# Performance work log

Hardware: AMD Instinct MI355X
Metric: run time of the kernel (lower is better)

Reference implementation:

```python
import jax, jax.numpy as jnp
import numpy as np

HEADS = 4
DIM_HEAD = 32
CHUNK = 1024
GROUPS = 8
EPS = 1e-5


def setup_inputs() -> dict:
    key = jax.random.key(0)
    k1, k2, k3 = jax.random.split(key, 3)
    b, dim, h, w = 8, 64, 96, 96
    inner = HEADS * DIM_HEAD  # 128
    x = jax.random.normal(k1, (b, dim, h, w), dtype=jnp.float32)
    W_qkv = jax.random.normal(k2, (3 * inner, dim), dtype=jnp.float32) * (1.0 / np.sqrt(dim))
    W_out = jax.random.normal(k3, (dim, inner), dtype=jnp.float32) * (1.0 / np.sqrt(inner))
    b_out = jnp.zeros((dim,), dtype=jnp.float32)
    gamma = jnp.ones((dim,), dtype=jnp.float32)
    beta = jnp.zeros((dim,), dtype=jnp.float32)
    return {"x": x, "W_qkv": W_qkv, "W_out": W_out, "b_out": b_out,
            "gamma": gamma, "beta": beta}


def reference(x, W_qkv, W_out, b_out, gamma, beta):
    b, c, h, w = x.shape
    n = h * w
    nch = n // CHUNK  # number of full chunks (n chosen divisible by CHUNK)
    d = DIM_HEAD
    BH = b * HEADS

    # 1x1 conv (no bias) == matmul over channel dim
    xf = x.reshape(b, c, n)
    qkv = jnp.einsum('oc,bcn->bon', W_qkv, xf)          # [b, 3*inner, n]
    q, k, v = jnp.split(qkv, 3, axis=1)                  # each [b, inner, n]

    def chunkify(t):
        # [b, inner, n] -> [BH, nch, d, CHUNK]; slicing i:i+CHUNK on last axis
        # equals reshaping n -> (nch, CHUNK) in order.
        return t.reshape(BH, d, nch, CHUNK).transpose(0, 2, 1, 3)

    qc, kc, vc = chunkify(q), chunkify(k), chunkify(v)

    qs = jax.nn.softmax(qc, axis=-1)  # softmax over chunk spatial positions
    ks = jax.nn.softmax(kc, axis=-2)  # softmax over head channels

    # context = k_chunk^T @ v_chunk : [BH, nch, CHUNK, CHUNK]
    ctx = jnp.einsum('gkdi,gkdj->gkij', ks, vc)
    # chunk_out = q_chunk @ context : [BH, nch, d, CHUNK]
    out = jnp.einsum('gkdi,gkij->gkdj', qs, ctx)

    # concat chunks back along spatial dim, reshape to image layout
    out = out.transpose(0, 2, 1, 3).reshape(b, HEADS * d, h, w)

    # to_out: 1x1 conv with bias, then GroupNorm(8, dim)
    y = jnp.einsum('oc,bchw->bohw', W_out, out) + b_out[None, :, None, None]

    yg = y.reshape(b, GROUPS, c // GROUPS, h, w)
    mu = jnp.mean(yg, axis=(2, 3, 4), keepdims=True)
    var = jnp.var(yg, axis=(2, 3, 4), keepdims=True)
    yn = ((yg - mu) * jax.lax.rsqrt(var + EPS)).reshape(b, c, h, w)
    return yn * gamma[None, :, None, None] + beta[None, :, None, None]
```

## Files before the change

kernel.cpp:

```cpp
#include <hip/hip_runtime.h>
#include <hip/hip_bf16.h>

#define N_POS 9216
#define NCHUNK 9
#define BATCH 8
#define CDIM 64
#define HEADS 4
#define EPS 1e-5f

#define PPART_SZ ((size_t)32 * NCHUNK * 1024)
#define NPART 8
#define UBF_BYTES ((size_t)BATCH * NCHUNK * 64 * 128 * 2)
#define WBF_BYTES ((size_t)384 * 64 * 2)

typedef __attribute__((ext_vector_type(8))) short short8;
typedef __attribute__((ext_vector_type(4))) float f32x4;

static __device__ inline unsigned pk2(float a, float b) {
    __hip_bfloat162 h2(__float2bfloat16(a), __float2bfloat16(b));
    return *reinterpret_cast<unsigned*>(&h2);
}
static __device__ inline float bf2f(short s) {
    union { unsigned u; float f; } c; c.u = ((unsigned)(unsigned short)s) << 16; return c.f;
}

__global__ __launch_bounds__(256) void wprep_kernel(const float* __restrict__ Wqkv,
        __hip_bfloat16* __restrict__ wbf, float* __restrict__ stats) {
    int i = blockIdx.x * 256 + threadIdx.x;
    if (i < 6144) {
        float4 v = ((const float4*)Wqkv)[i];
        uint2 u; u.x = pk2(v.x, v.y); u.y = pk2(v.z, v.w);
        ((uint2*)wbf)[i] = u;
    }
    if (i < 128) stats[i] = 0.f;
}

__global__ __launch_bounds__(256) void qkp_kernel(const float* __restrict__ x,
        const __hip_bfloat16* __restrict__ wbf, float* __restrict__ Pparts) {
    int bx = blockIdx.x;
    int b  = blockIdx.y;
    int ck = bx >> 3, pt = bx & 7;
    __shared__ __align__(16) char lraw[36864];
    __hip_bfloat16 (*xs)[72]  = (__hip_bfloat16(*)[72])lraw;
    __hip_bfloat16 (*skT)[72] = (__hip_bfloat16(*)[72])lraw;
    int t = threadIdx.x, w = t >> 6, l = t & 63;
    int l15 = l & 15, quad = l >> 4;

    f32x4 pac[2][2];
    pac[0][0] = (f32x4){0,0,0,0}; pac[0][1] = (f32x4){0,0,0,0};
    pac[1][0] = (f32x4){0,0,0,0}; pac[1][1] = (f32x4){0,0,0,0};

    for (int half = 0; half < 2; ++half) {
        int n0 = bx * 128 + half * 64;
        {
            int p = t & 63, cbase = (t >> 6) * 16;
            const float* xb = x + (size_t)b * CDIM * N_POS + n0 + p;
            #pragma unroll
            for (int j = 0; j < 16; j += 4) {
                float v0 = xb[(size_t)(cbase + j + 0) * N_POS];
                float v1 = xb[(size_t)(cbase + j + 1) * N_POS];
                float v2 = xb[(size_t)(cbase + j + 2) * N_POS];
                float v3 = xb[(size_t)(cbase + j + 3) * N_POS];
                uint2 u; u.x = pk2(v0, v1); u.y = pk2(v2, v3);
                *reinterpret_cast<uint2*>(&xs[p][cbase + j]) = u;
            }
        }
        __syncthreads();

        f32x4 acc[4][4];
        #pragma unroll
        for (int mt = 0; mt < 4; ++mt)
            #pragma unroll
            for (int nt = 0; nt < 4; ++nt) acc[mt][nt] = (f32x4){0.f, 0.f, 0.f, 0.f};
        #pragma unroll
        for (int ks = 0; ks < 2; ++ks) {
            int k0 = ks * 32 + quad * 8;
            short8 av[4];
            #pragma unroll
            for (int mt = 0; mt < 4; ++mt)
                av[mt] = *reinterpret_cast<const short8*>(&xs[mt * 16 + l15][k0]);
            #pragma unroll
            for (int nt = 0; nt < 4; ++nt) {
                short8 bw = *reinterpret_cast<const short8*>(wbf + (size_t)(w * 64 + nt * 16 + l15) * 64 + k0);
                #pragma unroll
                for (int mt = 0; mt < 4; ++mt)
                    acc[mt][nt] = __builtin_amdgcn_mfma_f32_16x16x32_bf16(av[mt], bw, acc[mt][nt], 0, 0, 0);
            }
        }
        __syncthreads();

        if (w < 2) {
            #pragma unroll
            for (int nt = 0; nt < 4; ++nt) {
                int ch = w * 64 + nt * 16 + l15;
                #pragma unroll
                for (int mt = 0; mt < 4; ++mt) {
                    uint2 u;
                    u.x = pk2(__expf(acc[mt][nt][0]), __expf(acc[mt][nt][1]));
                    u.y = pk2(__expf(acc[mt][nt][2]), __expf(acc[mt][nt][3]));
                    *reinterpret_cast<uint2*>(&skT[ch][mt * 16 + quad * 4]) = u;
                }
            }
        } else {
            #pragma unroll
            for (int nt = 0; nt < 4; ++nt) {
                int ch = w * 64 + nt * 16 + l15;
                #pragma unroll
                for (int mt = 0; mt < 4; ++mt) {
                    uint2 u;
                    u.x = pk2(acc[mt][nt][0], acc[mt][nt][1]);
                    u.y = pk2(acc[mt][nt][2], acc[mt][nt][3]);
                    *reinterpret_cast<uint2*>(&skT[ch][mt * 16 + quad * 4]) = u;
                }
            }
        }
        __syncthreads();

        {
            int p = t & 63, h = t >> 6;
            float kr[32]; float mx = -1e30f;
            #pragma unroll
            for (int d = 0; d < 32; ++d) { kr[d] = bf2f(*(const short*)&skT[128 + h * 32 + d][p]); mx = fmaxf(mx, kr[d]); }
            float s = 0.f;
            #pragma unroll
            for (int d = 0; d < 32; ++d) { kr[d] = __expf(kr[d] - mx); s += kr[d]; }
            float is = 1.f / s;
            #pragma unroll
            for (int d = 0; d < 32; ++d) skT[128 + h * 32 + d][p] = __float2bfloat16(kr[d] * is);
        }
        __syncthreads();

        #pragma unroll
        for (int step = 0; step < 2; ++step) {
            int k0 = step * 32 + quad * 8;
            short8 bk[2];
            #pragma unroll
            for (int nt = 0; nt < 2; ++nt)
                bk[nt] = *reinterpret_cast<const short8*>(&skT[128 + w * 32 + nt * 16 + l15][k0]);
            #pragma unroll
            for (int mt = 0; mt < 2; ++mt) {
                short8 aq = *reinterpret_cast<const short8*>(&skT[w * 32 + mt * 16 + l15][k0]);
                pac[mt][0] = __builtin_amdgcn_mfma_f32_16x16x32_bf16(aq, bk[0], pac[mt][0], 0, 0, 0);
                pac[mt][1] = __builtin_amdgcn_mfma_f32_16x16x32_bf16(aq, bk[1], pac[mt][1], 0, 0, 0);
            }
        }
        __syncthreads();
    }

    float* Pp = Pparts + (size_t)pt * PPART_SZ + ((size_t)(b * 4 + w) * NCHUNK + ck) * 1024;
    #pragma unroll
    for (int mt = 0; mt < 2; ++mt)
        #pragma unroll
        for (int nt = 0; nt < 2; ++nt)
            #pragma unroll
            for (int r = 0; r < 4; ++r)
                Pp[(mt * 16 + quad * 4 + r) * 32 + nt * 16 + l15] = pac[mt][nt][r];
}

__global__ __launch_bounds__(256) void umat_kernel(const float* __restrict__ Wout,
        const float* __restrict__ Pparts, __hip_bfloat16* __restrict__ Ubf) {
    int ck = blockIdx.x, b = blockIdx.y, h = blockIdx.z;
    int bh = b * 4 + h;
    int t = threadIdx.x;
    __shared__ float Pl[32][32];
    __shared__ float iZ[32];
    size_t base4 = ((size_t)bh * NCHUNK + ck) * 256;
    {
        const float4* P0 = (const float4*)Pparts + base4 + t;
        float4 s = (float4){0.f, 0.f, 0.f, 0.f};
        #pragma unroll
        for (int j = 0; j < NPART; ++j) {
            float4 a = P0[j * (PPART_SZ / 4)];
            s.x += a.x; s.y += a.y; s.z += a.z; s.w += a.w;
        }
        ((float4*)Pl)[t] = s;
    }
    __syncthreads();
    if (t < 32) {
        float s = 0.f;
        #pragma unroll
        for (int c = 0; c < 32; ++c) s += Pl[t][c];
        iZ[t] = 1.f / s;
    }
    __syncthreads();
    int o = t & 63, wv = t >> 6;
    float wz[32];
    {
        const float4* wr = (const float4*)(Wout + (size_t)o * 128 + h * 32);
        #pragma unroll
        for (int j = 0; j < 8; ++j) {
            float4 f = wr[j];
            wz[j*4+0] = f.x * iZ[j*4+0]; wz[j*4+1] = f.y * iZ[j*4+1];
            wz[j*4+2] = f.z * iZ[j*4+2]; wz[j*4+3] = f.w * iZ[j*4+3];
        }
    }
    float ua[8];
    #pragma unroll
    for (int j = 0; j < 8; ++j) ua[j] = 0.f;
    for (int d = 0; d < 32; ++d) {
        float wd = wz[d];
        #pragma unroll
        for (int j = 0; j < 8; ++j) ua[j] += wd * Pl[d][wv * 8 + j];
    }
    uint4 up;
    up.x = pk2(ua[0], ua[1]); up.y = pk2(ua[2], ua[3]);
    up.z = pk2(ua[4], ua[5]); up.w = pk2(ua[6], ua[7]);
    __hip_bfloat16* Up = Ubf + ((size_t)(b * NCHUNK + ck) * 64 + o) * 128 + h * 32 + wv * 8;
    *reinterpret_cast<uint4*>(Up) = up;
}

__global__ __launch_bounds__(256) void vy_kernel(const float* __restrict__ x,
        const __hip_bfloat16* __restrict__ wbf, const __hip_bfloat16* __restrict__ Ubf,
        const float* __restrict__ bout, __hip_bfloat16* __restrict__ ybf,
        float* __restrict__ stats) {
    int bx = blockIdx.x;
    int b  = blockIdx.y;
    int ck = bx >> 3;
    int n0 = bx * 128;
    __shared__ __align__(16) char lraw[34816];
    __hip_bfloat16 (*xs)[72]    = (__hip_bfloat16(*)[72])lraw;
    __hip_bfloat16 (*vbuf)[136] = (__hip_bfloat16(*)[136])lraw;
    __shared__ float gsum[8], gsq[8];
    int t = threadIdx.x, w = t >> 6, l = t & 63;
    int l15 = l & 15, quad = l >> 4;
    if (t < 8) { gsum[t] = 0.f; gsq[t] = 0.f; }

    {
        int p = t & 127, cbase = (t >> 7) * 32;
        const float* xb = x + (size_t)b * CDIM * N_POS + n0 + p;
        #pragma unroll
        for (int j = 0; j < 32; j += 4) {
            float v0 = xb[(size_t)(cbase + j + 0) * N_POS];
            float v1 = xb[(size_t)(cbase + j + 1) * N_POS];
            float v2 = xb[(size_t)(cbase + j + 2) * N_POS];
            float v3 = xb[(size_t)(cbase + j + 3) * N_POS];
            uint2 u; u.x = pk2(v0, v1); u.y = pk2(v2, v3);
            *reinterpret_cast<uint2*>(&xs[p][cbase + j]) = u;
        }
    }
    __syncthreads();

    int nw = w * 32;
    {
        f32x4 vacc[8][2];
        #pragma unroll
        for (int mt = 0; mt < 8; ++mt) { vacc[mt][0] = (f32x4){0,0,0,0}; vacc[mt][1] = (f32x4){0,0,0,0}; }
        #pragma unroll
        for (int ks = 0; ks < 2; ++ks) {
            int k0 = ks * 32 + quad * 8;
            short8 bfr[2];
            #pragma unroll
            for (int nt = 0; nt < 2; ++nt)
                bfr[nt] = *reinterpret_cast<const short8*>(&xs[nw + nt * 16 + l15][k0]);
            #pragma unroll
            for (int mt = 0; mt < 8; ++mt) {
                short8 afr = *reinterpret_cast<const short8*>(wbf + (size_t)(256 + mt * 16 + l15) * 64 + k0);
                vacc[mt][0] = __builtin_amdgcn_mfma_f32_16x16x32_bf16(afr, bfr[0], vacc[mt][0], 0, 0, 0);
                vacc[mt][1] = __builtin_amdgcn_mfma_f32_16x16x32_bf16(afr, bfr[1], vacc[mt][1], 0, 0, 0);
            }
        }
        __syncthreads();

        #pragma unroll
        for (int mt = 0; mt < 8; ++mt)
            #pragma unroll
            for (int nt = 0; nt < 2; ++nt) {
                int p = nw + nt * 16 + l15;
                uint2 u;
                u.x = pk2(vacc[mt][nt][0], vacc[mt][nt][1]);
                u.y = pk2(vacc[mt][nt][2], vacc[mt][nt][3]);
                *reinterpret_cast<uint2*>(&vbuf[p][mt * 16 + quad * 4]) = u;
            }
    }
    __syncthreads();

    const __hip_bfloat16* Ub = Ubf + (size_t)(b * NCHUNK + ck) * 64 * 128;
    f32x4 acc[4][2];
    #pragma unroll
    for (int mt = 0; mt < 4; ++mt) { acc[mt][0] = (f32x4){0,0,0,0}; acc[mt][1] = (f32x4){0,0,0,0}; }
    #pragma unroll
    for (int ks = 0; ks < 4; ++ks) {
        int k0 = ks * 32 + quad * 8;
        short8 bf[2];
        #pragma unroll
        for (int nt = 0; nt < 2; ++nt)
            bf[nt] = *reinterpret_cast<const short8*>(&vbuf[nw + nt * 16 + l15][k0]);
        #pragma unroll
        for (int mt = 0; mt < 4; ++mt) {
            short8 af = *reinterpret_cast<const short8*>(Ub + (size_t)(mt * 16 + l15) * 128 + k0);
            acc[mt][0] = __builtin_amdgcn_mfma_f32_16x16x32_bf16(af, bf[0], acc[mt][0], 0, 0, 0);
            acc[mt][1] = __builtin_amdgcn_mfma_f32_16x16x32_bf16(af, bf[1], acc[mt][1], 0, 0, 0);
        }
    }
    float gsl[4], gql[4];
    #pragma unroll
    for (int mt = 0; mt < 4; ++mt) { gsl[mt] = 0.f; gql[mt] = 0.f; }
    __hip_bfloat16* yb = ybf + (size_t)b * CDIM * N_POS;
    int nbase = n0 + nw;
    #pragma unroll
    for (int mt = 0; mt < 4; ++mt) {
        float4 bo = *reinterpret_cast<const float4*>(bout + mt * 16 + quad * 4);
        const float* bop = reinterpret_cast<const float*>(&bo);
        #pragma unroll
        for (int nt = 0; nt < 2; ++nt) {
            int n = nbase + nt * 16 + l15;
            #pragma unroll
            for (int r = 0; r < 4; ++r) {
                int o = mt * 16 + quad * 4 + r;
                float val = acc[mt][nt][r] + bop[r];
                yb[(size_t)o * N_POS + n] = __float2bfloat16(val);
                gsl[mt] += val; gql[mt] += val * val;
            }
        }
    }
    #pragma unroll
    for (int off = 16; off >= 1; off >>= 1) {
        #pragma unroll
        for (int mt = 0; mt < 4; ++mt) {
            gsl[mt] += __shfl_xor(gsl[mt], off, 64);
            gql[mt] += __shfl_xor(gql[mt], off, 64);
        }
    }
    if (l == 0 || l == 32) {
        int qh = quad >> 1;
        #pragma unroll
        for (int mt = 0; mt < 4; ++mt) {
            atomicAdd(&gsum[2 * mt + qh], gsl[mt]);
            atomicAdd(&gsq[2 * mt + qh], gql[mt]);
        }
    }
    __syncthreads();
    if (t < 8) {
        atomicAdd(&stats[(b * 8 + t) * 2],     gsum[t]);
        atomicAdd(&stats[(b * 8 + t) * 2 + 1], gsq[t]);
    }
}

__global__ __launch_bounds__(256) void gn_kernel(const __hip_bfloat16* __restrict__ ybf,
        float* __restrict__ out, const float* __restrict__ stats,
        const float* __restrict__ gamma, const float* __restrict__ beta) {
    int bc = blockIdx.y;
    int c = bc & 63, b = bc >> 6;
    int g = c >> 3;
    float s = stats[(b * 8 + g) * 2], q = stats[(b * 8 + g) * 2 + 1];
    const float invN = 1.f / (8.f * N_POS);
    float mean = s * invN;
    float var = q * invN - mean * mean;
    float sc = rsqrtf(var + EPS);
    float ga = gamma[c] * sc;
    float be = beta[c] - mean * sc * gamma[c];
    size_t base = ((size_t)b * CDIM + c) * N_POS + (size_t)(blockIdx.x * 256 + threadIdx.x) * 4;
    uint2 u = *reinterpret_cast<const uint2*>(ybf + base);
    float4 v;
    v.x = bf2f((short)(u.x & 0xffff)); v.y = bf2f((short)(u.x >> 16));
    v.z = bf2f((short)(u.y & 0xffff)); v.w = bf2f((short)(u.y >> 16));
    v.x = v.x * ga + be; v.y = v.y * ga + be; v.z = v.z * ga + be; v.w = v.w * ga + be;
    *reinterpret_cast<float4*>(out + base) = v;
}

extern "C" void kernel_launch(void* const* d_in, const int* in_sizes, int n_in,
                              void* d_out, int out_size, void* d_ws, size_t ws_size,
                              hipStream_t stream) {
    const float* x     = (const float*)d_in[0];
    const float* Wqkv  = (const float*)d_in[1];
    const float* Wout  = (const float*)d_in[2];
    const float* bout  = (const float*)d_in[3];
    const float* gamma = (const float*)d_in[4];
    const float* beta  = (const float*)d_in[5];
    float* out = (float*)d_out;

    float* stats  = (float*)d_ws;
    float* Pparts = stats + 128;
    __hip_bfloat16* Ubf = (__hip_bfloat16*)(Pparts + NPART * PPART_SZ);
    __hip_bfloat16* wbf = (__hip_bfloat16*)((char*)Ubf + UBF_BYTES);
    __hip_bfloat16* ybf = (__hip_bfloat16*)((char*)wbf + WBF_BYTES);

    wprep_kernel<<<dim3(24), 256, 0, stream>>>(Wqkv, wbf, stats);
    qkp_kernel<<<dim3(72, BATCH), 256, 0, stream>>>(x, wbf, Pparts);
    umat_kernel<<<dim3(NCHUNK, BATCH, HEADS), 256, 0, stream>>>(Wout, Pparts, Ubf);
    vy_kernel<<<dim3(72, BATCH), 256, 0, stream>>>(x, wbf, Ubf, bout, ybf, stats);
    gn_kernel<<<dim3(9, 512), 256, 0, stream>>>(ybf, out, stats, gamma, beta);
}
```

Baseline: 123.0 us.

## Fold value projection into per-chunk output matrix to skip V computation

```diff
diff --git a/kernel.cpp b/kernel.cpp
--- a/kernel.cpp
+++ b/kernel.cpp
@@ -10,7 +10,7 @@
 
 #define PPART_SZ ((size_t)32 * NCHUNK * 1024)
 #define NPART 8
-#define UBF_BYTES ((size_t)BATCH * NCHUNK * 64 * 128 * 2)
+#define MP_SLICE ((size_t)(BATCH * NCHUNK) * 4096)
 #define WBF_BYTES ((size_t)384 * 64 * 2)
 
 typedef __attribute__((ext_vector_type(8))) short short8;
@@ -158,12 +158,15 @@
 }
 
 __global__ __launch_bounds__(256) void umat_kernel(const float* __restrict__ Wout,
-        const float* __restrict__ Pparts, __hip_bfloat16* __restrict__ Ubf) {
+        const float* __restrict__ Wqkv, const float* __restrict__ Pparts,
+        float* __restrict__ Mp) {
     int ck = blockIdx.x, b = blockIdx.y, h = blockIdx.z;
     int bh = b * 4 + h;
     int t = threadIdx.x;
     __shared__ float Pl[32][32];
     __shared__ float iZ[32];
+    __shared__ float Ul[64][33];
+    __shared__ float Wvh[32][68];
     size_t base4 = ((size_t)bh * NCHUNK + ck) * 256;
     {
         const float4* P0 = (const float4*)Pparts + base4 + t;
@@ -174,6 +177,13 @@
             s.x += a.x; s.y += a.y; s.z += a.z; s.w += a.w;
         }
         ((float4*)Pl)[t] = s;
+    }
+    {
+        int e = t >> 3, cq = t & 7;
+        const float4* wr = (const float4*)(Wqkv + (size_t)(256 + h * 32 + e) * 64 + cq * 8);
+        float4 a0 = wr[0], a1 = wr[1];
+        *reinterpret_cast<float4*>(&Wvh[e][cq * 8])     = a0;
+        *reinterpret_cast<float4*>(&Wvh[e][cq * 8 + 4]) = a1;
     }
     __syncthreads();
     if (t < 32) {
@@ -202,24 +212,41 @@
         #pragma unroll
         for (int j = 0; j < 8; ++j) ua[j] += wd * Pl[d][wv * 8 + j];
     }
-    uint4 up;
-    up.x = pk2(ua[0], ua[1]); up.y = pk2(ua[2], ua[3]);
-    up.z = pk2(ua[4], ua[5]); up.w = pk2(ua[6], ua[7]);
-    __hip_bfloat16* Up = Ubf + ((size_t)(b * NCHUNK + ck) * 64 + o) * 128 + h * 32 + wv * 8;
-    *reinterpret_cast<uint4*>(Up) = up;
-}
-
-__global__ __launch_bounds__(256) void vy_kernel(const float* __restrict__ x,
-        const __hip_bfloat16* __restrict__ wbf, const __hip_bfloat16* __restrict__ Ubf,
-        const float* __restrict__ bout, __hip_bfloat16* __restrict__ ybf,
-        float* __restrict__ stats) {
+    #pragma unroll
+    for (int j = 0; j < 8; ++j) Ul[o][wv * 8 + j] = ua[j];
+    __syncthreads();
+
+    float macc[16];
+    #pragma unroll
+    for (int j = 0; j < 16; ++j) macc[j] = 0.f;
+    for (int e = 0; e < 32; ++e) {
+        float u = Ul[o][e];
+        const float4* wvp = reinterpret_cast<const float4*>(&Wvh[e][wv * 16]);
+        #pragma unroll
+        for (int q = 0; q < 4; ++q) {
+            float4 f = wvp[q];
+            macc[q*4+0] += u * f.x; macc[q*4+1] += u * f.y;
+            macc[q*4+2] += u * f.z; macc[q*4+3] += u * f.w;
+        }
+    }
+    float* mp = Mp + (size_t)h * MP_SLICE + ((size_t)(b * NCHUNK + ck)) * 4096
+              + (size_t)o * 64 + wv * 16;
+    #pragma unroll
+    for (int q = 0; q < 4; ++q) {
+        float4 f; f.x = macc[q*4+0]; f.y = macc[q*4+1]; f.z = macc[q*4+2]; f.w = macc[q*4+3];
+        reinterpret_cast<float4*>(mp)[q] = f;
+    }
+}
+
+__global__ __launch_bounds__(256) void y_kernel(const float* __restrict__ x,
+        const float* __restrict__ Mp, const float* __restrict__ bout,
+        __hip_bfloat16* __restrict__ ybf, float* __restrict__ stats) {
     int bx = blockIdx.x;
     int b  = blockIdx.y;
     int ck = bx >> 3;
     int n0 = bx * 128;
-    __shared__ __align__(16) char lraw[34816];
-    __hip_bfloat16 (*xs)[72]    = (__hip_bfloat16(*)[72])lraw;
-    __hip_bfloat16 (*vbuf)[136] = (__hip_bfloat16(*)[136])lraw;
+    __shared__ __align__(16) __hip_bfloat16 xs[128][72];
+    __shared__ __align__(16) __hip_bfloat16 Ml[64][72];
     __shared__ float gsum[8], gsq[8];
     int t = threadIdx.x, w = t >> 6, l = t & 63;
     int l15 = l & 15, quad = l >> 4;
@@ -238,56 +265,46 @@
             *reinterpret_cast<uint2*>(&xs[p][cbase + j]) = u;
         }
     }
+    {
+        int o = t >> 2, cs = (t & 3) * 16;
+        const float* mb = Mp + ((size_t)(b * NCHUNK + ck)) * 4096 + (size_t)o * 64 + cs;
+        float m[16];
+        #pragma unroll
+        for (int q = 0; q < 4; ++q) {
+            float4 f = reinterpret_cast<const float4*>(mb)[q];
+            m[q*4+0] = f.x; m[q*4+1] = f.y; m[q*4+2] = f.z; m[q*4+3] = f.w;
+        }
+        #pragma unroll
+        for (int h = 1; h < 4; ++h) {
+            const float* mh = mb + h * MP_SLICE;
+            #pragma unroll
+            for (int q = 0; q < 4; ++q) {
+                float4 f = reinterpret_cast<const float4*>(mh)[q];
+                m[q*4+0] += f.x; m[q*4+1] += f.y; m[q*4+2] += f.z; m[q*4+3] += f.w;
+            }
+        }
+        #pragma unroll
+        for (int q = 0; q < 4; ++q) {
+            uint2 u; u.x = pk2(m[q*4+0], m[q*4+1]); u.y = pk2(m[q*4+2], m[q*4+3]);
+            *reinterpret_cast<uint2*>(&Ml[o][cs + q * 4]) = u;
+        }
+    }
     __syncthreads();
 
     int nw = w * 32;
-    {
-        f32x4 vacc[8][2];
-        #pragma unroll
-        for (int mt = 0; mt < 8; ++mt) { vacc[mt][0] = (f32x4){0,0,0,0}; vacc[mt][1] = (f32x4){0,0,0,0}; }
-        #pragma unroll
-        for (int ks = 0; ks < 2; ++ks) {
-            int k0 = ks * 32 + quad * 8;
-            short8 bfr[2];
-            #pragma unroll
-            for (int nt = 0; nt < 2; ++nt)
-                bfr[nt] = *reinterpret_cast<const short8*>(&xs[nw + nt * 16 + l15][k0]);
-            #pragma unroll
-            for (int mt = 0; mt < 8; ++mt) {
-                short8 afr = *reinterpret_cast<const short8*>(wbf + (size_t)(256 + mt * 16 + l15) * 64 + k0);
-                vacc[mt][0] = __builtin_amdgcn_mfma_f32_16x16x32_bf16(afr, bfr[0], vacc[mt][0], 0, 0, 0);
-                vacc[mt][1] = __builtin_amdgcn_mfma_f32_16x16x32_bf16(afr, bfr[1], vacc[mt][1], 0, 0, 0);
-            }
-        }
-        __syncthreads();
-
-        #pragma unroll
-        for (int mt = 0; mt < 8; ++mt)
-            #pragma unroll
-            for (int nt = 0; nt < 2; ++nt) {
-                int p = nw + nt * 16 + l15;
-                uint2 u;
-                u.x = pk2(vacc[mt][nt][0], vacc[mt][nt][1]);
-                u.y = pk2(vacc[mt][nt][2], vacc[mt][nt][3]);
-                *reinterpret_cast<uint2*>(&vbuf[p][mt * 16 + quad * 4]) = u;
-            }
-    }
-    __syncthreads();
-
-    const __hip_bfloat16* Ub = Ubf + (size_t)(b * NCHUNK + ck) * 64 * 128;
     f32x4 acc[4][2];
     #pragma unroll
     for (int mt = 0; mt < 4; ++mt) { acc[mt][0] = (f32x4){0,0,0,0}; acc[mt][1] = (f32x4){0,0,0,0}; }
     #pragma unroll
-    for (int ks = 0; ks < 4; ++ks) {
+    for (int ks = 0; ks < 2; ++ks) {
         int k0 = ks * 32 + quad * 8;
         short8 bf[2];
         #pragma unroll
         for (int nt = 0; nt < 2; ++nt)
-            bf[nt] = *reinterpret_cast<const short8*>(&vbuf[nw + nt * 16 + l15][k0]);
+            bf[nt] = *reinterpret_cast<const short8*>(&xs[nw + nt * 16 + l15][k0]);
         #pragma unroll
         for (int mt = 0; mt < 4; ++mt) {
-            short8 af = *reinterpret_cast<const short8*>(Ub + (size_t)(mt * 16 + l15) * 128 + k0);
+            short8 af = *reinterpret_cast<const short8*>(&Ml[mt * 16 + l15][k0]);
             acc[mt][0] = __builtin_amdgcn_mfma_f32_16x16x32_bf16(af, bf[0], acc[mt][0], 0, 0, 0);
             acc[mt][1] = __builtin_amdgcn_mfma_f32_16x16x32_bf16(af, bf[1], acc[mt][1], 0, 0, 0);
         }
@@ -371,13 +388,13 @@
 
     float* stats  = (float*)d_ws;
     float* Pparts = stats + 128;
-    __hip_bfloat16* Ubf = (__hip_bfloat16*)(Pparts + NPART * PPART_SZ);
-    __hip_bfloat16* wbf = (__hip_bfloat16*)((char*)Ubf + UBF_BYTES);
+    float* Mp     = Pparts + NPART * PPART_SZ;
+    __hip_bfloat16* wbf = (__hip_bfloat16*)(Mp + 4 * MP_SLICE);
     __hip_bfloat16* ybf = (__hip_bfloat16*)((char*)wbf + WBF_BYTES);
 
     wprep_kernel<<<dim3(24), 256, 0, stream>>>(Wqkv, wbf, stats);
     qkp_kernel<<<dim3(72, BATCH), 256, 0, stream>>>(x, wbf, Pparts);
-    umat_kernel<<<dim3(NCHUNK, BATCH, HEADS), 256, 0, stream>>>(Wout, Pparts, Ubf);
-    vy_kernel<<<dim3(72, BATCH), 256, 0, stream>>>(x, wbf, Ubf, bout, ybf, stats);
+    umat_kernel<<<dim3(NCHUNK, BATCH, HEADS), 256, 0, stream>>>(Wout, Wqkv, Pparts, Mp);
+    y_kernel<<<dim3(72, BATCH), 256, 0, stream>>>(x, Mp, bout, ybf, stats);
     gn_kernel<<<dim3(9, 512), 256, 0, stream>>>(ybf, out, stats, gamma, beta);
 }
```

Result: no change. 125.4 us (+1.9%).
